# Performance work log

Hardware: AMD Instinct MI355X
Metric: run time of the kernel (lower is better)

Reference implementation:

```python
import jax, jax.numpy as jnp
import numpy as np

CUTOFF = 5.0
B, A, N, G, F = 32, 256, 64, 50, 128


def _ssp(v):
    # shifted softplus used by SchNet filter network
    return jax.nn.softplus(v) - jnp.log(2.0).astype(v.dtype)


def setup_inputs() -> dict:
    key = jax.random.key(0)
    ks = jax.random.split(key, 8)
    x = jax.random.normal(ks[0], (B, A, F), dtype=jnp.float32)
    r_ij = jax.random.uniform(ks[1], (B, A, N), dtype=jnp.float32) * 4.5
    f_ij = jax.random.normal(ks[2], (B, A, N, G), dtype=jnp.float32)
    pairwise_mask = jnp.ones((B, A, N), dtype=jnp.float32)
    neighbors = jax.random.randint(ks[3], (B, A, N), 0, A, dtype=jnp.int64)
    in2f_w = jax.random.normal(ks[4], (F, F), dtype=jnp.float32) / np.sqrt(F)
    fw1 = jax.random.normal(ks[5], (G, F), dtype=jnp.float32) / np.sqrt(G)
    fb1 = jnp.zeros((F,), dtype=jnp.float32)
    fw2 = jax.random.normal(ks[6], (F, F), dtype=jnp.float32) / np.sqrt(F)
    fb2 = jnp.zeros((F,), dtype=jnp.float32)
    return {"x": x, "r_ij": r_ij, "f_ij": f_ij, "pairwise_mask": pairwise_mask,
            "neighbors": neighbors, "in2f_w": in2f_w, "fw1": fw1, "fb1": fb1,
            "fw2": fw2, "fb2": fb2}


def reference(x, r_ij, f_ij, pairwise_mask, neighbors, in2f_w, fw1, fb1, fw2, fb2):
    # filter network: Dense(G->F, shifted softplus) -> Dense(F->F, linear)
    W = _ssp(jnp.einsum('bang,gf->banf', f_ij, fw1) + fb1)
    W = jnp.einsum('banh,hf->banf', W, fw2) + fb2          # (B,A,N,F)
    # cosine cutoff
    C = 0.5 * (jnp.cos(r_ij * (jnp.pi / CUTOFF)) + 1.0)
    C = C * (r_ij < CUTOFF).astype(r_ij.dtype)
    W = W * C[..., None]
    # in2f dense (no bias)
    y = jnp.einsum('bai,if->baf', x, in2f_w)               # (B,A,F)
    # gather neighbor features along atom axis
    b_idx = jnp.arange(B)[:, None, None]
    y_nbh = y[b_idx, neighbors]                             # (B,A,N,F)
    # elementwise filter multiply + masked sum over neighbor axis
    out = jnp.sum(y_nbh * W * pairwise_mask[..., None], axis=2)  # (B,A,F)
    return out
```

## Files before the change

### kernel.cpp

```cpp
#include <hip/hip_runtime.h>
#include <math.h>

#define Bdim 32
#define Adim 256
#define Ndim 64
#define Gdim 50
#define Fdim 128

typedef __attribute__((ext_vector_type(8)))  short short8;
typedef __attribute__((ext_vector_type(16))) float floatx16;

__device__ __forceinline__ unsigned short f2bf_u(float x) {
    unsigned u = __builtin_bit_cast(unsigned, x);
    return (unsigned short)((u + 0x7FFFu + ((u >> 16) & 1u)) >> 16);
}
__device__ __forceinline__ unsigned pk2bf(float a, float b) {
    return (unsigned)f2bf_u(a) | ((unsigned)f2bf_u(b) << 16);
}
__device__ __forceinline__ float bf2f(unsigned short v) {
    return __builtin_bit_cast(float, ((unsigned)v) << 16);
}
__device__ __forceinline__ float sspf(float v) {
    float t = __expf(-fabsf(v));
    return fmaxf(v, 0.0f) + __logf(1.0f + t) - 0.69314718056f;
}
__device__ __forceinline__ short8 mk8(unsigned a, unsigned b, unsigned c, unsigned d) {
    union { unsigned u[4]; short8 s; } t;
    t.u[0] = a; t.u[1] = b; t.u[2] = c; t.u[3] = d;
    return t.s;
}

__global__ __launch_bounds__(256) void in2f_mfma(const float* __restrict__ x,
                                                 const float* __restrict__ w,
                                                 unsigned short* __restrict__ y) {
    __shared__ __align__(16) short sWT[128 * 132];
    const int tid = threadIdx.x;
    for (int idx = tid; idx < 128 * 128; idx += 256) {
        int i = idx >> 7, f = idx & 127;
        sWT[f * 132 + i] = (short)f2bf_u(w[idx]);
    }
    __syncthreads();
    const int wv = tid >> 6, lane = tid & 63, lm = lane & 31, lh = lane >> 5;
    const int rbase = blockIdx.x * 128 + wv * 32;
    floatx16 acc[4];
#pragma unroll
    for (int jt = 0; jt < 4; ++jt)
#pragma unroll
        for (int e = 0; e < 16; ++e) acc[jt][e] = 0.0f;

    const float* xr = x + (size_t)(rbase + lm) * 128;
#pragma unroll
    for (int ks = 0; ks < 8; ++ks) {
        int g0 = ks * 16 + lh * 8;
        float4 q0 = *(const float4*)(xr + g0);
        float4 q1 = *(const float4*)(xr + g0 + 4);
        short8 a = mk8(pk2bf(q0.x, q0.y), pk2bf(q0.z, q0.w),
                       pk2bf(q1.x, q1.y), pk2bf(q1.z, q1.w));
#pragma unroll
        for (int jt = 0; jt < 4; ++jt) {
            const short* bp = &sWT[(jt * 32 + lm) * 132 + g0];
            uint2 b0 = *(const uint2*)bp;
            uint2 b1 = *(const uint2*)(bp + 4);
            acc[jt] = __builtin_amdgcn_mfma_f32_32x32x16_bf16(
                a, mk8(b0.x, b0.y, b1.x, b1.y), acc[jt], 0, 0, 0);
        }
    }
#pragma unroll
    for (int jt = 0; jt < 4; ++jt)
#pragma unroll
        for (int r = 0; r < 16; ++r) {
            int row = rbase + (r & 3) + 8 * (r >> 2) + 4 * lh;
            y[(size_t)row * 128 + jt * 32 + lm] = f2bf_u(acc[jt][r]);
        }
}

__global__ __launch_bounds__(256, 3) void cfconv_mfma2(
    const float* __restrict__ r_ij, const float* __restrict__ f_ij,
    const float* __restrict__ mask, const int* __restrict__ nbr,
    const float* __restrict__ fw1, const float* __restrict__ fb1,
    const float* __restrict__ fw2, const float* __restrict__ fb2,
    const unsigned short* __restrict__ ybf, float* __restrict__ out)
{
    __shared__ __align__(16) short sFw1[128 * 68];
    __shared__ __align__(16) short sFw2[128 * 132];
    __shared__ __align__(16) float sCm[128];
    __shared__ __align__(16) int   sNbr[128];
    __shared__ __align__(16) float sRed[4 * 128];

    const int tid = threadIdx.x, wv = tid >> 6, lane = tid & 63;
    const int lm = lane & 31, lh = lane >> 5;

    for (int idx = tid; idx < Gdim * 128; idx += 256) {
        int g = idx >> 7, f = idx & 127;
        sFw1[f * 68 + g] = (short)f2bf_u(fw1[idx]);
    }
    for (int idx = tid; idx < 128 * 14; idx += 256) {
        int f = idx / 14, g = Gdim + idx % 14;
        sFw1[f * 68 + g] = (g == Gdim) ? (short)f2bf_u(fb1[f]) : (short)0;
    }
    for (int idx = tid; idx < 128 * 128; idx += 256) {
        int h = idx >> 7, f = idx & 127;
        sFw2[f * 132 + h] = (short)f2bf_u(fw2[idx]);
    }
    float fb2v[4];
#pragma unroll
    for (int jt = 0; jt < 4; ++jt) fb2v[jt] = fb2[jt * 32 + lm];

    for (int it = 0; it < 4; ++it) {
        const int sp = blockIdx.x + 1024 * it;
        if (tid < 128) {
            int site = sp * 2 + (tid >> 6), n = tid & 63;
            float r = r_ij[(size_t)site * Ndim + n];
            float c = 0.5f * (__cosf(r * 0.62831853071796f) + 1.0f);
            c = (r < 5.0f) ? c : 0.0f;
            sCm[tid]  = c * mask[(size_t)site * Ndim + n];
            sNbr[tid] = nbr[(size_t)site * Ndim + n];
        }
        const int ps = sp * 2 + (wv >> 1);
        const int nb = (wv & 1) * 32;
        const float* fr = f_ij + ((size_t)ps * Ndim + nb + lm) * Gdim;
        unsigned bfr[4][4];
#pragma unroll
        for (int ks = 0; ks < 3; ++ks) {
            int g0 = ks * 16 + lh * 8;
            float2 q0 = *(const float2*)(fr + g0);
            float2 q1 = *(const float2*)(fr + g0 + 2);
            float2 q2 = *(const float2*)(fr + g0 + 4);
            float2 q3 = *(const float2*)(fr + g0 + 6);
            bfr[ks][0] = pk2bf(q0.x, q0.y); bfr[ks][1] = pk2bf(q1.x, q1.y);
            bfr[ks][2] = pk2bf(q2.x, q2.y); bfr[ks][3] = pk2bf(q3.x, q3.y);
        }
        if (lh == 0) {
            float2 q = *(const float2*)(fr + 48);
            bfr[3][0] = pk2bf(q.x, q.y); bfr[3][1] = 0x00003F80u;
            bfr[3][2] = 0u; bfr[3][3] = 0u;
        } else { bfr[3][0] = bfr[3][1] = bfr[3][2] = bfr[3][3] = 0u; }
        __syncthreads();

        unsigned A2[8][4];
#pragma unroll
        for (int ft = 0; ft < 4; ++ft) {
            floatx16 a1;
#pragma unroll
            for (int e = 0; e < 16; ++e) a1[e] = 0.0f;
#pragma unroll
            for (int ks = 0; ks < 4; ++ks) {
                const short* ap = &sFw1[(ft * 32 + lm) * 68 + ks * 16 + lh * 8];
                uint2 a0 = *(const uint2*)ap;
                uint2 a1v = *(const uint2*)(ap + 4);
                a1 = __builtin_amdgcn_mfma_f32_32x32x16_bf16(
                    mk8(a0.x, a0.y, a1v.x, a1v.y),
                    mk8(bfr[ks][0], bfr[ks][1], bfr[ks][2], bfr[ks][3]),
                    a1, 0, 0, 0);
            }
            unsigned P[8], X[8];
#pragma unroll
            for (int q = 0; q < 8; ++q)
                P[q] = pk2bf(sspf(a1[2 * q]), sspf(a1[2 * q + 1]));
#pragma unroll
            for (int q = 0; q < 8; ++q) X[q] = (unsigned)__shfl_xor((int)P[q], 32);
            A2[2*ft][0]   = lh ? X[2] : P[0];  A2[2*ft][1]   = lh ? X[3] : P[1];
            A2[2*ft][2]   = lh ? P[2] : X[0];  A2[2*ft][3]   = lh ? P[3] : X[1];
            A2[2*ft+1][0] = lh ? X[6] : P[4];  A2[2*ft+1][1] = lh ? X[7] : P[5];
            A2[2*ft+1][2] = lh ? P[6] : X[4];  A2[2*ft+1][3] = lh ? P[7] : X[5];
        }

        floatx16 acc2[4];
#pragma unroll
        for (int jt = 0; jt < 4; ++jt)
#pragma unroll
            for (int e = 0; e < 16; ++e) acc2[jt][e] = 0.0f;
#pragma unroll
        for (int ks = 0; ks < 8; ++ks) {
            short8 a = mk8(A2[ks][0], A2[ks][1], A2[ks][2], A2[ks][3]);
#pragma unroll
            for (int jt = 0; jt < 4; ++jt) {
                const short* bp = &sFw2[(jt * 32 + lm) * 132 + ks * 16 + lh * 8];
                uint2 b0 = *(const uint2*)bp;
                uint2 b1 = *(const uint2*)(bp + 4);
                acc2[jt] = __builtin_amdgcn_mfma_f32_32x32x16_bf16(
                    a, mk8(b0.x, b0.y, b1.x, b1.y), acc2[jt], 0, 0, 0);
            }
        }

        float cmv[16]; int nbv[16];
#pragma unroll
        for (int rq = 0; rq < 4; ++rq) {
            float4 c4 = *(const float4*)&sCm[wv * 32 + rq * 8 + lh * 4];
            int4   n4 = *(const int4*)&sNbr[wv * 32 + rq * 8 + lh * 4];
            cmv[rq*4+0] = c4.x; cmv[rq*4+1] = c4.y; cmv[rq*4+2] = c4.z; cmv[rq*4+3] = c4.w;
            nbv[rq*4+0] = n4.x; nbv[rq*4+1] = n4.y; nbv[rq*4+2] = n4.z; nbv[rq*4+3] = n4.w;
        }
        const int bofs = (ps >> 8) * Adim;
        float part[4] = {0.f, 0.f, 0.f, 0.f};
#pragma unroll
        for (int r = 0; r < 16; ++r) {
            float cm = cmv[r];
            const unsigned short* yr = ybf + (size_t)(bofs + nbv[r]) * 128;
#pragma unroll
            for (int jt = 0; jt < 4; ++jt) {
                float yv = bf2f(yr[jt * 32 + lm]);
                part[jt] += (acc2[jt][r] + fb2v[jt]) * cm * yv;
            }
        }
#pragma unroll
        for (int jt = 0; jt < 4; ++jt) {
            float s = part[jt] + __shfl_xor(part[jt], 32);
            if (lh == 0) sRed[wv * 128 + jt * 32 + lm] = s;
        }
        __syncthreads();
        {
            int s = tid >> 7, f = tid & 127;
            out[(size_t)(sp * 2 + s) * 128 + f] =
                sRed[(2 * s) * 128 + f] + sRed[(2 * s + 1) * 128 + f];
        }
    }
}

extern "C" void kernel_launch(void* const* d_in, const int* in_sizes, int n_in,
                              void* d_out, int out_size, void* d_ws, size_t ws_size,
                              hipStream_t stream) {
    const float* x      = (const float*)d_in[0];
    const float* r_ij   = (const float*)d_in[1];
    const float* f_ij   = (const float*)d_in[2];
    const float* mask   = (const float*)d_in[3];
    const int*   nbr    = (const int*)d_in[4];
    const float* in2f_w = (const float*)d_in[5];
    const float* fw1    = (const float*)d_in[6];
    const float* fb1    = (const float*)d_in[7];
    const float* fw2    = (const float*)d_in[8];
    const float* fb2    = (const float*)d_in[9];
    float* out = (float*)d_out;
    unsigned short* y = (unsigned short*)d_ws;

    in2f_mfma<<<64, 256, 0, stream>>>(x, in2f_w, y);
    cfconv_mfma2<<<1024, 256, 0, stream>>>(r_ij, f_ij, mask, nbr,
                                           fw1, fb1, fw2, fb2, y, out);
}
```

Baseline: 261.8 us.

## Stage f_ij and x tiles through LDS with coalesced loads before MFMA

The main kernel now loads each block's f_ij tile with coalesced float2 loads, converts it to bf16 into shared memory (with the bias/padding columns preset once), and reads MFMA B fragments from LDS. Previously each lane did strided per-row global loads. The in2f kernel likewise stages its x tile in LDS and uses vectorized loads for the weight transpose. bf16 conversion now goes through the HIP intrinsic. The extra LDS use lowers the occupancy hint from 3 to 2 blocks per CU and adds a round trip through shared memory.

```diff
diff --git a/kernel.cpp b/kernel.cpp
--- a/kernel.cpp
+++ b/kernel.cpp
@@ -1,4 +1,5 @@
 #include <hip/hip_runtime.h>
+#include <hip/hip_bf16.h>
 #include <math.h>
 
 #define Bdim 32
@@ -11,8 +12,8 @@
 typedef __attribute__((ext_vector_type(16))) float floatx16;
 
 __device__ __forceinline__ unsigned short f2bf_u(float x) {
-    unsigned u = __builtin_bit_cast(unsigned, x);
-    return (unsigned short)((u + 0x7FFFu + ((u >> 16) & 1u)) >> 16);
+    __hip_bfloat16 h = __float2bfloat16(x);
+    return __builtin_bit_cast(unsigned short, h);
 }
 __device__ __forceinline__ unsigned pk2bf(float a, float b) {
     return (unsigned)f2bf_u(a) | ((unsigned)f2bf_u(b) << 16);
@@ -30,32 +31,47 @@
     return t.s;
 }
 
-__global__ __launch_bounds__(256) void in2f_mfma(const float* __restrict__ x,
-                                                 const float* __restrict__ w,
-                                                 unsigned short* __restrict__ y) {
-    __shared__ __align__(16) short sWT[128 * 132];
+__global__ __launch_bounds__(256) void in2f_mfma2(const float* __restrict__ x,
+                                                  const float* __restrict__ w,
+                                                  unsigned short* __restrict__ y) {
+    __shared__ short sWT[128 * 132];
+    __shared__ short sX [128 * 132];
     const int tid = threadIdx.x;
-    for (int idx = tid; idx < 128 * 128; idx += 256) {
-        int i = idx >> 7, f = idx & 127;
-        sWT[f * 132 + i] = (short)f2bf_u(w[idx]);
+
+#pragma unroll 4
+    for (int k = 0; k < 32; ++k) {
+        int idx = tid + k * 256;
+        float2 v = *(const float2*)(w + 2 * idx);
+        int i = idx >> 6;
+        int f = (2 * idx) & 127;
+        sWT[f * 132 + i]       = (short)f2bf_u(v.x);
+        sWT[(f + 1) * 132 + i] = (short)f2bf_u(v.y);
+    }
+    const float* xb = x + (size_t)blockIdx.x * (128 * 128);
+#pragma unroll 4
+    for (int k = 0; k < 32; ++k) {
+        int idx = tid + k * 256;
+        float2 v = *(const float2*)(xb + 2 * idx);
+        int row = idx >> 6;
+        int i = (2 * idx) & 127;
+        *(unsigned*)&sX[row * 132 + i] = pk2bf(v.x, v.y);
     }
     __syncthreads();
+
     const int wv = tid >> 6, lane = tid & 63, lm = lane & 31, lh = lane >> 5;
-    const int rbase = blockIdx.x * 128 + wv * 32;
     floatx16 acc[4];
 #pragma unroll
     for (int jt = 0; jt < 4; ++jt)
 #pragma unroll
         for (int e = 0; e < 16; ++e) acc[jt][e] = 0.0f;
 
-    const float* xr = x + (size_t)(rbase + lm) * 128;
 #pragma unroll
     for (int ks = 0; ks < 8; ++ks) {
         int g0 = ks * 16 + lh * 8;
-        float4 q0 = *(const float4*)(xr + g0);
-        float4 q1 = *(const float4*)(xr + g0 + 4);
-        short8 a = mk8(pk2bf(q0.x, q0.y), pk2bf(q0.z, q0.w),
-                       pk2bf(q1.x, q1.y), pk2bf(q1.z, q1.w));
+        const short* ap = &sX[(wv * 32 + lm) * 132 + g0];
+        uint2 a0 = *(const uint2*)ap;
+        uint2 a1 = *(const uint2*)(ap + 4);
+        short8 a = mk8(a0.x, a0.y, a1.x, a1.y);
 #pragma unroll
         for (int jt = 0; jt < 4; ++jt) {
             const short* bp = &sWT[(jt * 32 + lm) * 132 + g0];
@@ -65,6 +81,7 @@
                 a, mk8(b0.x, b0.y, b1.x, b1.y), acc[jt], 0, 0, 0);
         }
     }
+    const int rbase = blockIdx.x * 128 + wv * 32;
 #pragma unroll
     for (int jt = 0; jt < 4; ++jt)
 #pragma unroll
@@ -74,40 +91,63 @@
         }
 }
 
-__global__ __launch_bounds__(256, 3) void cfconv_mfma2(
+#define SF1 68
+#define SF2 132
+#define SFI 60
+
+__global__ __launch_bounds__(256, 2) void cfconv_mfma3(
     const float* __restrict__ r_ij, const float* __restrict__ f_ij,
     const float* __restrict__ mask, const int* __restrict__ nbr,
     const float* __restrict__ fw1, const float* __restrict__ fb1,
     const float* __restrict__ fw2, const float* __restrict__ fb2,
     const unsigned short* __restrict__ ybf, float* __restrict__ out)
 {
-    __shared__ __align__(16) short sFw1[128 * 68];
-    __shared__ __align__(16) short sFw2[128 * 132];
-    __shared__ __align__(16) float sCm[128];
-    __shared__ __align__(16) int   sNbr[128];
-    __shared__ __align__(16) float sRed[4 * 128];
+    __shared__ short sFw1[128 * SF1];
+    __shared__ short sFw2[128 * SF2];
+    __shared__ short sFij[128 * SFI + 16];
+    __shared__ float sCm[128];
+    __shared__ int   sNbr[128];
+    __shared__ float sRed[4 * 128];
 
     const int tid = threadIdx.x, wv = tid >> 6, lane = tid & 63;
     const int lm = lane & 31, lh = lane >> 5;
 
     for (int idx = tid; idx < Gdim * 128; idx += 256) {
         int g = idx >> 7, f = idx & 127;
-        sFw1[f * 68 + g] = (short)f2bf_u(fw1[idx]);
+        sFw1[f * SF1 + g] = (short)f2bf_u(fw1[idx]);
     }
     for (int idx = tid; idx < 128 * 14; idx += 256) {
         int f = idx / 14, g = Gdim + idx % 14;
-        sFw1[f * 68 + g] = (g == Gdim) ? (short)f2bf_u(fb1[f]) : (short)0;
+        sFw1[f * SF1 + g] = (g == Gdim) ? (short)f2bf_u(fb1[f]) : (short)0;
     }
     for (int idx = tid; idx < 128 * 128; idx += 256) {
         int h = idx >> 7, f = idx & 127;
-        sFw2[f * 132 + h] = (short)f2bf_u(fw2[idx]);
-    }
+        sFw2[f * SF2 + h] = (short)f2bf_u(fw2[idx]);
+    }
+    for (int idx = tid; idx < 128 * 5; idx += 256) {
+        int row = idx / 5, k = idx - row * 5;
+        *(unsigned*)&sFij[row * SFI + 50 + 2 * k] = (k == 0) ? 0x00003F80u : 0u;
+    }
+    if (tid < 8) *(unsigned*)&sFij[128 * SFI + 2 * tid] = 0u;
+
     float fb2v[4];
 #pragma unroll
     for (int jt = 0; jt < 4; ++jt) fb2v[jt] = fb2[jt * 32 + lm];
 
     for (int it = 0; it < 4; ++it) {
         const int sp = blockIdx.x + 1024 * it;
+
+        const float* fp = f_ij + (size_t)sp * (2 * Ndim * Gdim);
+#pragma unroll
+        for (int k = 0; k < 13; ++k) {
+            int idx = tid + k * 256;
+            if (idx < 3200) {
+                float2 v = *(const float2*)(fp + 2 * idx);
+                int row = idx / 25;
+                int g   = 2 * idx - row * 50;
+                *(unsigned*)&sFij[row * SFI + g] = pk2bf(v.x, v.y);
+            }
+        }
         if (tid < 128) {
             int site = sp * 2 + (tid >> 6), n = tid & 63;
             float r = r_ij[(size_t)site * Ndim + n];
@@ -116,27 +156,9 @@
             sCm[tid]  = c * mask[(size_t)site * Ndim + n];
             sNbr[tid] = nbr[(size_t)site * Ndim + n];
         }
-        const int ps = sp * 2 + (wv >> 1);
-        const int nb = (wv & 1) * 32;
-        const float* fr = f_ij + ((size_t)ps * Ndim + nb + lm) * Gdim;
-        unsigned bfr[4][4];
-#pragma unroll
-        for (int ks = 0; ks < 3; ++ks) {
-            int g0 = ks * 16 + lh * 8;
-            float2 q0 = *(const float2*)(fr + g0);
-            float2 q1 = *(const float2*)(fr + g0 + 2);
-            float2 q2 = *(const float2*)(fr + g0 + 4);
-            float2 q3 = *(const float2*)(fr + g0 + 6);
-            bfr[ks][0] = pk2bf(q0.x, q0.y); bfr[ks][1] = pk2bf(q1.x, q1.y);
-            bfr[ks][2] = pk2bf(q2.x, q2.y); bfr[ks][3] = pk2bf(q3.x, q3.y);
-        }
-        if (lh == 0) {
-            float2 q = *(const float2*)(fr + 48);
-            bfr[3][0] = pk2bf(q.x, q.y); bfr[3][1] = 0x00003F80u;
-            bfr[3][2] = 0u; bfr[3][3] = 0u;
-        } else { bfr[3][0] = bfr[3][1] = bfr[3][2] = bfr[3][3] = 0u; }
         __syncthreads();
 
+        const int rowb = wv * 32;
         unsigned A2[8][4];
 #pragma unroll
         for (int ft = 0; ft < 4; ++ft) {
@@ -145,13 +167,16 @@
             for (int e = 0; e < 16; ++e) a1[e] = 0.0f;
 #pragma unroll
             for (int ks = 0; ks < 4; ++ks) {
-                const short* ap = &sFw1[(ft * 32 + lm) * 68 + ks * 16 + lh * 8];
+                int g0 = ks * 16 + lh * 8;
+                const short* ap = &sFw1[(ft * 32 + lm) * SF1 + g0];
                 uint2 a0 = *(const uint2*)ap;
                 uint2 a1v = *(const uint2*)(ap + 4);
+                const short* bp = &sFij[(rowb + lm) * SFI + g0];
+                uint2 b0 = *(const uint2*)bp;
+                uint2 b1v = *(const uint2*)(bp + 4);
                 a1 = __builtin_amdgcn_mfma_f32_32x32x16_bf16(
                     mk8(a0.x, a0.y, a1v.x, a1v.y),
-                    mk8(bfr[ks][0], bfr[ks][1], bfr[ks][2], bfr[ks][3]),
-                    a1, 0, 0, 0);
+                    mk8(b0.x, b0.y, b1v.x, b1v.y), a1, 0, 0, 0);
             }
             unsigned P[8], X[8];
 #pragma unroll
@@ -175,7 +200,7 @@
             short8 a = mk8(A2[ks][0], A2[ks][1], A2[ks][2], A2[ks][3]);
 #pragma unroll
             for (int jt = 0; jt < 4; ++jt) {
-                const short* bp = &sFw2[(jt * 32 + lm) * 132 + ks * 16 + lh * 8];
+                const short* bp = &sFw2[(jt * 32 + lm) * SF2 + ks * 16 + lh * 8];
                 uint2 b0 = *(const uint2*)bp;
                 uint2 b1 = *(const uint2*)(bp + 4);
                 acc2[jt] = __builtin_amdgcn_mfma_f32_32x32x16_bf16(
@@ -183,6 +208,7 @@
             }
         }
 
+        const int ps = sp * 2 + (wv >> 1);
         float cmv[16]; int nbv[16];
 #pragma unroll
         for (int rq = 0; rq < 4; ++rq) {
@@ -233,7 +259,7 @@
     float* out = (float*)d_out;
     unsigned short* y = (unsigned short*)d_ws;
 
-    in2f_mfma<<<64, 256, 0, stream>>>(x, in2f_w, y);
-    cfconv_mfma2<<<1024, 256, 0, stream>>>(r_ij, f_ij, mask, nbr,
+    in2f_mfma2<<<64, 256, 0, stream>>>(x, in2f_w, y);
+    cfconv_mfma3<<<1024, 256, 0, stream>>>(r_ij, f_ij, mask, nbr,
                                            fw1, fb1, fw2, fb2, y, out);
 }
```

Result: faster. 253.6 us (-3.1%).
